# Kernel tuning notes

Measured on AMD Instinct MI355X. Metric: run time of the kernel, lower is better.

Reference implementation:

```python
import jax, jax.numpy as jnp
import numpy as np

B, N, P, K = 4, 8192, 2048, 16
C_IN, C_OUT, DIMS = 64, 128, 3
C_MID = C_OUT // 4                      # 32 (C_in != 0 branch)
DM = min(int(np.ceil(C_OUT / C_IN)), 4) # 2, depth multiplier for SepConv
C_DENSE = C_OUT // 2                    # 64, dense-projected feature dim
C_CAT = C_MID + C_DENSE                 # 96, lifted + projected features


def setup_inputs() -> dict:
    key = jax.random.key(0)
    ks = jax.random.split(key, 12)
    g = lambda k, shape, fan: jax.random.normal(k, shape, jnp.float32) / np.sqrt(fan).astype(np.float32)
    return {
        "pts": jax.random.normal(ks[0], (B, N, DIMS), jnp.float32),
        "fts": jax.random.normal(ks[1], (B, N, C_IN), jnp.float32),
        # PointCNN.dense: Linear(C_in, C_out//2) + ELU
        "dense_W": g(ks[2], (C_IN, C_DENSE), C_IN), "dense_b": jnp.zeros((C_DENSE,), jnp.float32),
        # XConv.dense1/dense2: Linear(dims,C_mid)+ELU, Linear(C_mid,C_mid)+ELU
        "d1_W": g(ks[3], (DIMS, C_MID), DIMS), "d1_b": jnp.zeros((C_MID,), jnp.float32),
        "d2_W": g(ks[4], (C_MID, C_MID), C_MID), "d2_b": jnp.zeros((C_MID,), jnp.float32),
        # conv2d: Conv2d(dims, K*K, (1,K)) + ELU, weight (out, in, kW)
        "conv_W": g(ks[5], (K * K, DIMS, K), DIMS * K), "conv_b": jnp.zeros((K * K,), jnp.float32),
        # dep_conv1/2: depthwise Conv2d(K, K*K, (1,K), groups=K); weight (group, mult, kW)
        "dw1_W": g(ks[6], (K, K, K), K), "dw1_b": jnp.zeros((K, K), jnp.float32),
        "dw2_W": g(ks[7], (K, K, K), K), "dw2_b": jnp.zeros((K, K), jnp.float32),
        # end_conv SepConv: depthwise (C_CAT groups, DM mult, (1,K)) then pointwise 1x1 -> C_OUT, ELU
        "sep_dw_W": g(ks[8], (C_CAT, DM, K), K), "sep_dw_b": jnp.zeros((C_CAT, DM), jnp.float32),
        "sep_pw_W": g(ks[9], (C_OUT, C_CAT, DM), C_CAT * DM), "sep_pw_b": jnp.zeros((C_OUT,), jnp.float32),
    }


def _fps(pts, npoint):
    """Iterative farthest point sampling (deterministic start at index 0)."""
    b, n, _ = pts.shape
    dist0 = jnp.full((b, n), 1e10, pts.dtype)
    far0 = jnp.zeros((b,), jnp.int32)

    def step(carry, _):
        dist, far = carry
        centroid = jnp.take_along_axis(pts, far[:, None, None], axis=1)  # [B,1,3]
        d = jnp.sum((pts - centroid) ** 2, -1)                            # [B,N]
        dist = jnp.minimum(dist, d)
        return (dist, jnp.argmax(dist, -1).astype(jnp.int32)), far

    _, idx = jax.lax.scan(step, (dist0, far0), None, length=npoint)  # [P,B]
    idx = idx.T                                                       # [B,P]
    return jnp.take_along_axis(pts, idx[..., None], axis=1)          # [B,P,3]


def reference(pts, fts, dense_W, dense_b, d1_W, d1_b, d2_W, d2_b,
              conv_W, conv_b, dw1_W, dw1_b, dw2_W, dw2_b,
              sep_dw_W, sep_dw_b, sep_pw_W, sep_pw_b):
    rep_pts = _fps(pts, P)                                            # [B,P,3]
    fts_d = jax.nn.elu(fts @ dense_W + dense_b)                       # [B,N,64]
    # KNN: squared distances rep->all points, K smallest
    d2 = (jnp.sum(rep_pts ** 2, -1)[..., None]
          - 2.0 * jnp.einsum('npc,nqc->npq', rep_pts, pts)
          + jnp.sum(pts ** 2, -1)[:, None, :])                        # [B,P,N]
    _, idx = jax.lax.top_k(-d2, K)                                    # [B,P,K]
    bidx = jnp.arange(B)[:, None, None]
    pts_reg = pts[bidx, idx]                                          # [B,P,K,3]
    fts_reg = fts_d[bidx, idx]                                        # [B,P,K,64]
    # XConv
    pl = pts_reg - rep_pts[:, :, None, :]                             # local coords
    lift = jax.nn.elu(jax.nn.elu(pl @ d1_W + d1_b) @ d2_W + d2_b)     # [B,P,K,C_MID]
    fts_cat = jnp.concatenate([lift, fts_reg], -1)                    # [B,P,K,C_CAT]
    X = jax.nn.elu(jnp.einsum('npkc,ock->npo', pl, conv_W) + conv_b).reshape(B, P, K, K)
    # depthwise convs over neighbor axis (spatial dim collapses to 1 -> einsum)
    X = jax.nn.elu(jnp.einsum('npij,jmi->npjm', X, dw1_W) + dw1_b)
    X = jnp.einsum('npij,jmi->npjm', X, dw2_W) + dw2_b
    fts_X = jnp.einsum('npab,npbc->npac', X, fts_cat)                 # [B,P,K,C_CAT]
    # separable end conv: depthwise over K, pointwise to C_OUT, ELU
    d = jnp.einsum('npkc,cmk->npcm', fts_X, sep_dw_W) + sep_dw_b
    fts_p = jax.nn.elu(jnp.einsum('npcm,ocm->npo', d, sep_pw_W) + sep_pw_b)  # [B,P,C_OUT]
    return rep_pts, fts_p
```

## Files before the change

### kernel.cpp

```cpp
#include <hip/hip_runtime.h>

#define BB 4
#define NN 8192
#define PP 2048
#define KNB 16
#define CIN 64
#define COUT 128

__device__ __forceinline__ float elu(float x) { return x > 0.0f ? x : expm1f(x); }

__device__ __forceinline__ unsigned fkey(float d) {
    unsigned u = __float_as_uint(d);
    unsigned m = (unsigned)((int)u >> 31);
    return u ^ (m | 0x80000000u);
}

__device__ __forceinline__ float wave_max_dpp(float v) {
#define DPP_STEP(ctrl)                                                         \
    {                                                                          \
        int x = __float_as_int(v);                                             \
        int y = __builtin_amdgcn_update_dpp(x, x, (ctrl), 0xf, 0xf, false);    \
        v = fmaxf(v, __int_as_float(y));                                       \
    }
    DPP_STEP(0x111)
    DPP_STEP(0x112)
    DPP_STEP(0x114)
    DPP_STEP(0x118)
    DPP_STEP(0x142)
    DPP_STEP(0x143)
#undef DPP_STEP
    return __int_as_float(__builtin_amdgcn_readlane(__float_as_int(v), 63));
}

__device__ __forceinline__ unsigned wave_min_u32_dpp(unsigned v) {
#define DPP_STEP(ctrl)                                                         \
    {                                                                          \
        int y = __builtin_amdgcn_update_dpp((int)v, (int)v, (ctrl), 0xf, 0xf, false); \
        v = min(v, (unsigned)y);                                               \
    }
    DPP_STEP(0x111)
    DPP_STEP(0x112)
    DPP_STEP(0x114)
    DPP_STEP(0x118)
    DPP_STEP(0x142)
    DPP_STEP(0x143)
#undef DPP_STEP
    return (unsigned)__builtin_amdgcn_readlane((int)v, 63);
}

#define PREP_BLOCKS 64
#define DENSE_BASE (4 + PREP_BLOCKS)
#define TOTAL_BLOCKS (DENSE_BASE + BB * NN / 8)

__global__ __launch_bounds__(512) void fps_kernel(
    const float* __restrict__ pts, float* __restrict__ rep,
    const float* __restrict__ fts, const float* __restrict__ denseW,
    const float* __restrict__ denseb, float* __restrict__ ftsd,
    const float* __restrict__ convW, const float* __restrict__ dw1W,
    const float* __restrict__ dw2W, const float* __restrict__ sdwW,
    const float* __restrict__ spwW,
    float* __restrict__ convT, float* __restrict__ dw1T, float* __restrict__ dw2T,
    float* __restrict__ sdwT, float* __restrict__ spwT, float* __restrict__ ptsT) {
    const int bid = blockIdx.x;
    const int t = threadIdx.x;

    __shared__ float spx[NN];
    __shared__ float spy[NN];
    __shared__ float spz[NN];
    __shared__ unsigned long long partk[2][8];

    if (bid >= DENSE_BASE) {
        const int row = (bid - DENSE_BASE) * 8 + (t >> 6);
        const int c = t & 63;
        float v = fts[(size_t)row * 64 + c];
        float acc = denseb[c];
#pragma unroll 8
        for (int k = 0; k < 64; ++k) acc = fmaf(__shfl(v, k), denseW[k * 64 + c], acc);
        ftsd[(size_t)row * 64 + c] = elu(acc);
        return;
    }
    if (bid >= 4) {
        int i = (bid - 4) * 512 + t;
        if (i < 12288) {
            int k = i & 15, c = (i >> 4) % 3, o = i / 48;
            convT[(c * 16 + k) * 256 + o] = convW[i];
        }
        if (i < 4096) {
            int ii = i & 15, e = i >> 4;
            dw1T[ii * 256 + e] = dw1W[i];
            dw2T[ii * 256 + e] = dw2W[i];
        }
        if (i < 3072) {
            int k = i & 15, e = i >> 4;
            sdwT[k * 192 + e] = sdwW[i];
        }
        if (i < 24576) {
            int e2 = i % 192, o = i / 192;
            spwT[e2 * 128 + o] = spwW[i];
        }
        {
            int j = i & 8191, b2 = i >> 13;
#pragma unroll
            for (int d = 0; d < 3; ++d)
                ptsT[((size_t)b2 * 3 + d) * NN + j] = pts[((size_t)b2 * NN + j) * 3 + d];
        }
        return;
    }

    const int b = bid;
    const int lane = t & 63, wave = t >> 6;

    const float* pb = pts + (size_t)b * NN * 3;
    for (int i = t; i < NN; i += 512) {
        spx[i] = pb[3 * i + 0];
        spy[i] = pb[3 * i + 1];
        spz[i] = pb[3 * i + 2];
    }
    __syncthreads();

    float px[16], py[16], pz[16], dist[16];
#pragma unroll
    for (int r = 0; r < 16; ++r) {
        px[r] = spx[t * 16 + r];
        py[r] = spy[t * 16 + r];
        pz[r] = spz[t * 16 + r];
        dist[r] = 1e10f;
    }

    float cx = spx[0], cy = spy[0], cz = spz[0];
    if (t == 0) {
        rep[(size_t)b * PP * 3 + 0] = cx;
        rep[(size_t)b * PP * 3 + 1] = cy;
        rep[(size_t)b * PP * 3 + 2] = cz;
    }

    int buf = 0;
    for (int s = 1; s < PP; ++s) {
        float bv = -1.0f; int bi = 0;
#pragma unroll
        for (int r = 0; r < 16; ++r) {
            float dx = __fsub_rn(px[r], cx);
            float dy = __fsub_rn(py[r], cy);
            float dz = __fsub_rn(pz[r], cz);
            float d = __fadd_rn(__fadd_rn(__fmul_rn(dx, dx), __fmul_rn(dy, dy)), __fmul_rn(dz, dz));
            float nd = fminf(dist[r], d);
            dist[r] = nd;
            bool tk = nd > bv;
            bi = tk ? (t * 16 + r) : bi;
            bv = fmaxf(nd, bv);
        }

        float wmax = wave_max_dpp(bv);
        unsigned long long mask = __ballot(bv == wmax);
        int wl = __ffsll(mask) - 1;
        int wbi = __shfl(bi, wl);

        if (lane == 0)
            partk[buf][wave] = ((unsigned long long)__float_as_uint(wmax) << 32)
                             | (unsigned)(8191 - wbi);
        __syncthreads();

        unsigned long long kk = partk[buf][0];
#pragma unroll
        for (int q = 1; q < 8; ++q) {
            unsigned long long c = partk[buf][q];
            kk = c > kk ? c : kk;
        }
        int widx = 8191 - (int)(unsigned)(kk & 0xFFFFFFFFULL);
        cx = spx[widx]; cy = spy[widx]; cz = spz[widx];
        if (t == 0) {
            float* rp = rep + ((size_t)b * PP + s) * 3;
            rp[0] = cx; rp[1] = cy; rp[2] = cz;
        }
        buf ^= 1;
    }
}

__global__ __launch_bounds__(256) void knn_kernel(const float* __restrict__ ptsT,
                                                  const float* __restrict__ rep,
                                                  int* __restrict__ kidx) {
    const int wid = blockIdx.x * 4 + (threadIdx.x >> 6);
    const int lane = threadIdx.x & 63;
    const int b = wid >> 11;
    const float* pxT = ptsT + (size_t)b * 3 * NN;
    const float* pyT = pxT + NN;
    const float* pzT = pxT + 2 * NN;

    float rx = rep[(size_t)wid * 3 + 0];
    float ry = rep[(size_t)wid * 3 + 1];
    float rz = rep[(size_t)wid * 3 + 2];
    float a = __fadd_rn(__fadd_rn(__fmul_rn(rx, rx), __fmul_rn(ry, ry)), __fmul_rn(rz, rz));

    unsigned long long key[16];
#pragma unroll
    for (int s = 0; s < 16; ++s) key[s] = ~0ULL;

    unsigned tau = 0xFFFFFFFFu;
    int it = 0;
    for (int j = lane; j < NN; j += 64, ++it) {
        float qx = pxT[j], qy = pyT[j], qz = pzT[j];
        float cc = __fadd_rn(__fadd_rn(__fmul_rn(qx, qx), __fmul_rn(qy, qy)), __fmul_rn(qz, qz));
        float bs = __fadd_rn(__fadd_rn(__fmul_rn(rx, qx), __fmul_rn(ry, qy)), __fmul_rn(rz, qz));
        float d2 = __fadd_rn(__fsub_rn(a, __fmul_rn(2.0f, bs)), cc);
        unsigned fk = fkey(d2);
        if (fk <= tau) {
            unsigned long long nk = ((unsigned long long)fk << 32) | (unsigned)j;
            if (nk < key[15]) {
                key[15] = nk;
#pragma unroll
                for (int s2 = 15; s2 > 0; --s2) {
                    unsigned long long u = key[s2 - 1], w = key[s2];
                    bool sw = w < u;
                    key[s2 - 1] = sw ? w : u;
                    key[s2] = sw ? u : w;
                }
            }
        }
        if ((it & 7) == 7)
            tau = wave_min_u32_dpp((unsigned)(key[15] >> 32));
    }

    int outv = 0;
#pragma unroll 1
    for (int r = 0; r < 16; ++r) {
        unsigned long long h = key[0];
#pragma unroll
        for (int off = 1; off < 64; off <<= 1) {
            unsigned long long o = __shfl_xor(h, off);
            h = (o < h) ? o : h;
        }
        if (lane == r) outv = (int)(unsigned)(h & 0xFFFFFFFFull);
        if (key[0] == h) {
#pragma unroll
            for (int s2 = 0; s2 < 15; ++s2) key[s2] = key[s2 + 1];
            key[15] = ~0ULL;
        }
    }
    if (lane < 16) kidx[(size_t)wid * 16 + lane] = outv;
}

__global__ __launch_bounds__(128) void xconv_kernel(
    const float* __restrict__ pts, const float* __restrict__ rep,
    const float* __restrict__ ftsd, const int* __restrict__ kidx,
    const float* __restrict__ d1W, const float* __restrict__ d1b,
    const float* __restrict__ d2W, const float* __restrict__ d2b,
    const float* __restrict__ convT, const float* __restrict__ convb,
    const float* __restrict__ dw1T, const float* __restrict__ dw1b,
    const float* __restrict__ dw2T, const float* __restrict__ dw2b,
    const float* __restrict__ sdwT, const float* __restrict__ sdwb,
    const float* __restrict__ spwT, const float* __restrict__ spwb,
    float* __restrict__ outp) {
    const int bp = blockIdx.x;
    const int b = bp >> 11;
    const int t = threadIdx.x;
    const int c64 = t & 63;

    __shared__ float pl[16][3];
    __shared__ int nidx[16];
    __shared__ float fcat[16][96];
    __shared__ float A1[16][32];
    __shared__ float Xm[16][17];
    __shared__ float X2[16][17];
    __shared__ float X3[16][17];
    __shared__ float fX[16][97];
    __shared__ float dsep[192];

    if (t < 16) {
        int id = kidx[(size_t)bp * 16 + t];
        nidx[t] = id;
        const float* q = pts + ((size_t)b * NN + id) * 3;
        const float* rr = rep + (size_t)bp * 3;
        pl[t][0] = q[0] - rr[0];
        pl[t][1] = q[1] - rr[1];
        pl[t][2] = q[2] - rr[2];
    }
    __syncthreads();

#pragma unroll
    for (int it = 0; it < 8; ++it) {
        int k = (t >> 6) + it * 2;
        fcat[k][32 + c64] = ftsd[((size_t)b * NN + nidx[k]) * 64 + c64];
    }

#pragma unroll
    for (int r2 = 0; r2 < 4; ++r2) {
        int e = t + 128 * r2; int k = e >> 5, j = e & 31;
        float acc = d1b[j];
        acc = fmaf(pl[k][0], d1W[j], acc);
        acc = fmaf(pl[k][1], d1W[32 + j], acc);
        acc = fmaf(pl[k][2], d1W[64 + j], acc);
        A1[k][j] = elu(acc);
    }
    __syncthreads();

#pragma unroll
    for (int r2 = 0; r2 < 4; ++r2) {
        int e = t + 128 * r2; int k = e >> 5, j = e & 31;
        float acc = d2b[j];
#pragma unroll
        for (int c = 0; c < 32; ++c) acc = fmaf(A1[k][c], d2W[c * 32 + j], acc);
        fcat[k][j] = elu(acc);
    }
    __syncthreads();

    {
        float a0 = convb[t], a1 = convb[t + 128];
#pragma unroll
        for (int c = 0; c < 3; ++c)
#pragma unroll
            for (int k = 0; k < 16; ++k) {
                float p = pl[k][c];
                const float* w = convT + (c * 16 + k) * 256 + t;
                a0 = fmaf(p, w[0],   a0);
                a1 = fmaf(p, w[128], a1);
            }
        Xm[t >> 4][t & 15] = elu(a0);
        Xm[(t >> 4) + 8][t & 15] = elu(a1);
    }
    __syncthreads();

    {
        int m = t & 15, j0 = t >> 4;
        float a0 = dw1b[t], a1 = dw1b[t + 128];
#pragma unroll
        for (int i = 0; i < 16; ++i) {
            const float* w = dw1T + i * 256 + t;
            a0 = fmaf(Xm[i][j0],     w[0],   a0);
            a1 = fmaf(Xm[i][j0 + 8], w[128], a1);
        }
        X2[j0][m] = elu(a0); X2[j0 + 8][m] = elu(a1);
    }
    __syncthreads();

    {
        int m = t & 15, j0 = t >> 4;
        float a0 = dw2b[t], a1 = dw2b[t + 128];
#pragma unroll
        for (int i = 0; i < 16; ++i) {
            const float* w = dw2T + i * 256 + t;
            a0 = fmaf(X2[i][j0],     w[0],   a0);
            a1 = fmaf(X2[i][j0 + 8], w[128], a1);
        }
        X3[j0][m] = a0; X3[j0 + 8][m] = a1;
    }
    __syncthreads();

#pragma unroll
    for (int r2 = 0; r2 < 12; ++r2) {
        int e = t + 128 * r2; int a = e & 15, c = e >> 4;
        float acc = 0.0f;
#pragma unroll
        for (int q = 0; q < 16; ++q) acc = fmaf(X3[a][q], fcat[q][c], acc);
        fX[a][c] = acc;
    }
    __syncthreads();

#pragma unroll
    for (int r2 = 0; r2 < 2; ++r2) {
        int e = t + 128 * r2;
        if (e < 192) {
            int c = e >> 1;
            float acc = sdwb[e];
#pragma unroll
            for (int k = 0; k < 16; ++k) acc = fmaf(fX[k][c], sdwT[k * 192 + e], acc);
            dsep[e] = acc;
        }
    }
    __syncthreads();

    {
        float a0 = spwb[t];
#pragma unroll 16
        for (int e2 = 0; e2 < 192; ++e2)
            a0 = fmaf(dsep[e2], spwT[e2 * 128 + t], a0);
        outp[(size_t)bp * 128 + t] = elu(a0);
    }
}

extern "C" void kernel_launch(void* const* d_in, const int* in_sizes, int n_in,
                              void* d_out, int out_size, void* d_ws, size_t ws_size,
                              hipStream_t stream) {
    const float* pts    = (const float*)d_in[0];
    const float* fts    = (const float*)d_in[1];
    const float* denseW = (const float*)d_in[2];
    const float* denseb = (const float*)d_in[3];
    const float* d1W    = (const float*)d_in[4];
    const float* d1b    = (const float*)d_in[5];
    const float* d2W    = (const float*)d_in[6];
    const float* d2b    = (const float*)d_in[7];
    const float* convW  = (const float*)d_in[8];
    const float* convb  = (const float*)d_in[9];
    const float* dw1W   = (const float*)d_in[10];
    const float* dw1b   = (const float*)d_in[11];
    const float* dw2W   = (const float*)d_in[12];
    const float* dw2b   = (const float*)d_in[13];
    const float* sdwW   = (const float*)d_in[14];
    const float* sdwb   = (const float*)d_in[15];
    const float* spwW   = (const float*)d_in[16];
    const float* spwb   = (const float*)d_in[17];

    float* rep  = (float*)d_out;
    float* outp = (float*)d_out + (size_t)BB * PP * 3;

    float* ftsd = (float*)d_ws;
    int*   kidx = (int*)((char*)d_ws + (size_t)BB * NN * CIN * sizeof(float));
    float* wts  = (float*)((char*)d_ws + (size_t)BB * NN * CIN * sizeof(float)
                                       + (size_t)BB * PP * KNB * sizeof(int));
    float* convT = wts;
    float* dw1T  = wts + 12288;
    float* dw2T  = wts + 16384;
    float* sdwT  = wts + 20480;
    float* spwT  = wts + 23552;
    float* ptsT  = wts + 48128;

    fps_kernel<<<TOTAL_BLOCKS, 512, 0, stream>>>(pts, rep, fts, denseW, denseb, ftsd,
                                                 convW, dw1W, dw2W, sdwW, spwW,
                                                 convT, dw1T, dw2T, sdwT, spwT, ptsT);
    knn_kernel<<<BB * PP / 4, 256, 0, stream>>>(ptsT, rep, kidx);
    xconv_kernel<<<BB * PP, 128, 0, stream>>>(pts, rep, ftsd, kidx,
                                              d1W, d1b, d2W, d2b, convT, convb,
                                              dw1T, dw1b, dw2T, dw2b,
                                              sdwT, sdwb, spwT, spwb, outp);
}
```

Before: 2.269 ms.

## Fuse kNN into XConv kernel and use atomicMax reduction in FPS loop

Merges the kNN search and the XConv computation into one kernel. Each 128-thread block runs kNN for two points, one wave each, keeps the neighbor indices in shared memory, then processes both points' XConv in sequence. This removes a kernel launch and the global round trip for the neighbor indices. The FPS per-step reduction now has each wave atomicMax into a rotating triple-buffered shared slot, replacing the per-wave partial array and serial 8-way scan. Risks include shared atomic contention and lower parallelism in the XConv phase, since there are half as many blocks.

```diff
diff --git a/kernel.cpp b/kernel.cpp
--- a/kernel.cpp
+++ b/kernel.cpp
@@ -67,7 +67,7 @@
     __shared__ float spx[NN];
     __shared__ float spy[NN];
     __shared__ float spz[NN];
-    __shared__ unsigned long long partk[2][8];
+    __shared__ unsigned long long slots[3];
 
     if (bid >= DENSE_BASE) {
         const int row = (bid - DENSE_BASE) * 8 + (t >> 6);
@@ -108,7 +108,7 @@
     }
 
     const int b = bid;
-    const int lane = t & 63, wave = t >> 6;
+    const int lane = t & 63;
 
     const float* pb = pts + (size_t)b * NN * 3;
     for (int i = t; i < NN; i += 512) {
@@ -116,6 +116,7 @@
         spy[i] = pb[3 * i + 1];
         spz[i] = pb[3 * i + 2];
     }
+    if (t < 3) slots[t] = 0ULL;
     __syncthreads();
 
     float px[16], py[16], pz[16], dist[16];
@@ -134,7 +135,7 @@
         rep[(size_t)b * PP * 3 + 2] = cz;
     }
 
-    int buf = 0;
+    int cur = 1;
     for (int s = 1; s < PP; ++s) {
         float bv = -1.0f; int bi = 0;
 #pragma unroll
@@ -155,93 +156,28 @@
         int wl = __ffsll(mask) - 1;
         int wbi = __shfl(bi, wl);
 
+        int nxt = (cur == 2) ? 0 : cur + 1;
         if (lane == 0)
-            partk[buf][wave] = ((unsigned long long)__float_as_uint(wmax) << 32)
-                             | (unsigned)(8191 - wbi);
-        __syncthreads();
-
-        unsigned long long kk = partk[buf][0];
-#pragma unroll
-        for (int q = 1; q < 8; ++q) {
-            unsigned long long c = partk[buf][q];
-            kk = c > kk ? c : kk;
-        }
+            atomicMax((unsigned long long*)&slots[cur],
+                      ((unsigned long long)__float_as_uint(wmax) << 32)
+                      | (unsigned)(8191 - wbi));
+        if (t == 0) slots[nxt] = 0ULL;
+        __syncthreads();
+
+        unsigned long long kk = slots[cur];
         int widx = 8191 - (int)(unsigned)(kk & 0xFFFFFFFFULL);
         cx = spx[widx]; cy = spy[widx]; cz = spz[widx];
         if (t == 0) {
             float* rp = rep + ((size_t)b * PP + s) * 3;
             rp[0] = cx; rp[1] = cy; rp[2] = cz;
         }
-        buf ^= 1;
-    }
-}
-
-__global__ __launch_bounds__(256) void knn_kernel(const float* __restrict__ ptsT,
-                                                  const float* __restrict__ rep,
-                                                  int* __restrict__ kidx) {
-    const int wid = blockIdx.x * 4 + (threadIdx.x >> 6);
-    const int lane = threadIdx.x & 63;
-    const int b = wid >> 11;
-    const float* pxT = ptsT + (size_t)b * 3 * NN;
-    const float* pyT = pxT + NN;
-    const float* pzT = pxT + 2 * NN;
-
-    float rx = rep[(size_t)wid * 3 + 0];
-    float ry = rep[(size_t)wid * 3 + 1];
-    float rz = rep[(size_t)wid * 3 + 2];
-    float a = __fadd_rn(__fadd_rn(__fmul_rn(rx, rx), __fmul_rn(ry, ry)), __fmul_rn(rz, rz));
-
-    unsigned long long key[16];
-#pragma unroll
-    for (int s = 0; s < 16; ++s) key[s] = ~0ULL;
-
-    unsigned tau = 0xFFFFFFFFu;
-    int it = 0;
-    for (int j = lane; j < NN; j += 64, ++it) {
-        float qx = pxT[j], qy = pyT[j], qz = pzT[j];
-        float cc = __fadd_rn(__fadd_rn(__fmul_rn(qx, qx), __fmul_rn(qy, qy)), __fmul_rn(qz, qz));
-        float bs = __fadd_rn(__fadd_rn(__fmul_rn(rx, qx), __fmul_rn(ry, qy)), __fmul_rn(rz, qz));
-        float d2 = __fadd_rn(__fsub_rn(a, __fmul_rn(2.0f, bs)), cc);
-        unsigned fk = fkey(d2);
-        if (fk <= tau) {
-            unsigned long long nk = ((unsigned long long)fk << 32) | (unsigned)j;
-            if (nk < key[15]) {
-                key[15] = nk;
-#pragma unroll
-                for (int s2 = 15; s2 > 0; --s2) {
-                    unsigned long long u = key[s2 - 1], w = key[s2];
-                    bool sw = w < u;
-                    key[s2 - 1] = sw ? w : u;
-                    key[s2] = sw ? u : w;
-                }
-            }
-        }
-        if ((it & 7) == 7)
-            tau = wave_min_u32_dpp((unsigned)(key[15] >> 32));
-    }
-
-    int outv = 0;
-#pragma unroll 1
-    for (int r = 0; r < 16; ++r) {
-        unsigned long long h = key[0];
-#pragma unroll
-        for (int off = 1; off < 64; off <<= 1) {
-            unsigned long long o = __shfl_xor(h, off);
-            h = (o < h) ? o : h;
-        }
-        if (lane == r) outv = (int)(unsigned)(h & 0xFFFFFFFFull);
-        if (key[0] == h) {
-#pragma unroll
-            for (int s2 = 0; s2 < 15; ++s2) key[s2] = key[s2 + 1];
-            key[15] = ~0ULL;
-        }
-    }
-    if (lane < 16) kidx[(size_t)wid * 16 + lane] = outv;
-}
-
-__global__ __launch_bounds__(128) void xconv_kernel(
-    const float* __restrict__ pts, const float* __restrict__ rep,
-    const float* __restrict__ ftsd, const int* __restrict__ kidx,
+        cur = nxt;
+    }
+}
+
+__global__ __launch_bounds__(128) void knnxconv_kernel(
+    const float* __restrict__ ptsT, const float* __restrict__ pts,
+    const float* __restrict__ rep, const float* __restrict__ ftsd,
     const float* __restrict__ d1W, const float* __restrict__ d1b,
     const float* __restrict__ d2W, const float* __restrict__ d2b,
     const float* __restrict__ convT, const float* __restrict__ convb,
@@ -250,11 +186,12 @@
     const float* __restrict__ sdwT, const float* __restrict__ sdwb,
     const float* __restrict__ spwT, const float* __restrict__ spwb,
     float* __restrict__ outp) {
-    const int bp = blockIdx.x;
-    const int b = bp >> 11;
+    const int blk = blockIdx.x;
     const int t = threadIdx.x;
+    const int wv = t >> 6, lane = t & 63;
     const int c64 = t & 63;
 
+    __shared__ int kidx_l[2][16];
     __shared__ float pl[16][3];
     __shared__ int nidx[16];
     __shared__ float fcat[16][96];
@@ -265,115 +202,182 @@
     __shared__ float fX[16][97];
     __shared__ float dsep[192];
 
-    if (t < 16) {
-        int id = kidx[(size_t)bp * 16 + t];
-        nidx[t] = id;
-        const float* q = pts + ((size_t)b * NN + id) * 3;
-        const float* rr = rep + (size_t)bp * 3;
-        pl[t][0] = q[0] - rr[0];
-        pl[t][1] = q[1] - rr[1];
-        pl[t][2] = q[2] - rr[2];
-    }
-    __syncthreads();
-
-#pragma unroll
-    for (int it = 0; it < 8; ++it) {
-        int k = (t >> 6) + it * 2;
-        fcat[k][32 + c64] = ftsd[((size_t)b * NN + nidx[k]) * 64 + c64];
-    }
-
-#pragma unroll
-    for (int r2 = 0; r2 < 4; ++r2) {
-        int e = t + 128 * r2; int k = e >> 5, j = e & 31;
-        float acc = d1b[j];
-        acc = fmaf(pl[k][0], d1W[j], acc);
-        acc = fmaf(pl[k][1], d1W[32 + j], acc);
-        acc = fmaf(pl[k][2], d1W[64 + j], acc);
-        A1[k][j] = elu(acc);
-    }
-    __syncthreads();
-
-#pragma unroll
-    for (int r2 = 0; r2 < 4; ++r2) {
-        int e = t + 128 * r2; int k = e >> 5, j = e & 31;
-        float acc = d2b[j];
-#pragma unroll
-        for (int c = 0; c < 32; ++c) acc = fmaf(A1[k][c], d2W[c * 32 + j], acc);
-        fcat[k][j] = elu(acc);
-    }
-    __syncthreads();
-
     {
-        float a0 = convb[t], a1 = convb[t + 128];
-#pragma unroll
-        for (int c = 0; c < 3; ++c)
-#pragma unroll
-            for (int k = 0; k < 16; ++k) {
-                float p = pl[k][c];
-                const float* w = convT + (c * 16 + k) * 256 + t;
-                a0 = fmaf(p, w[0],   a0);
-                a1 = fmaf(p, w[128], a1);
-            }
-        Xm[t >> 4][t & 15] = elu(a0);
-        Xm[(t >> 4) + 8][t & 15] = elu(a1);
-    }
-    __syncthreads();
-
-    {
-        int m = t & 15, j0 = t >> 4;
-        float a0 = dw1b[t], a1 = dw1b[t + 128];
-#pragma unroll
-        for (int i = 0; i < 16; ++i) {
-            const float* w = dw1T + i * 256 + t;
-            a0 = fmaf(Xm[i][j0],     w[0],   a0);
-            a1 = fmaf(Xm[i][j0 + 8], w[128], a1);
-        }
-        X2[j0][m] = elu(a0); X2[j0 + 8][m] = elu(a1);
-    }
-    __syncthreads();
-
-    {
-        int m = t & 15, j0 = t >> 4;
-        float a0 = dw2b[t], a1 = dw2b[t + 128];
-#pragma unroll
-        for (int i = 0; i < 16; ++i) {
-            const float* w = dw2T + i * 256 + t;
-            a0 = fmaf(X2[i][j0],     w[0],   a0);
-            a1 = fmaf(X2[i][j0 + 8], w[128], a1);
-        }
-        X3[j0][m] = a0; X3[j0 + 8][m] = a1;
-    }
-    __syncthreads();
-
-#pragma unroll
-    for (int r2 = 0; r2 < 12; ++r2) {
-        int e = t + 128 * r2; int a = e & 15, c = e >> 4;
-        float acc = 0.0f;
-#pragma unroll
-        for (int q = 0; q < 16; ++q) acc = fmaf(X3[a][q], fcat[q][c], acc);
-        fX[a][c] = acc;
-    }
-    __syncthreads();
-
-#pragma unroll
-    for (int r2 = 0; r2 < 2; ++r2) {
-        int e = t + 128 * r2;
-        if (e < 192) {
-            int c = e >> 1;
-            float acc = sdwb[e];
-#pragma unroll
-            for (int k = 0; k < 16; ++k) acc = fmaf(fX[k][c], sdwT[k * 192 + e], acc);
-            dsep[e] = acc;
-        }
-    }
-    __syncthreads();
-
-    {
-        float a0 = spwb[t];
+        const int wid = blk * 2 + wv;
+        const int b = wid >> 11;
+        const float* pxT = ptsT + (size_t)b * 3 * NN;
+        const float* pyT = pxT + NN;
+        const float* pzT = pxT + 2 * NN;
+
+        float rx = rep[(size_t)wid * 3 + 0];
+        float ry = rep[(size_t)wid * 3 + 1];
+        float rz = rep[(size_t)wid * 3 + 2];
+        float a = __fadd_rn(__fadd_rn(__fmul_rn(rx, rx), __fmul_rn(ry, ry)), __fmul_rn(rz, rz));
+
+        unsigned long long key[16];
+#pragma unroll
+        for (int s = 0; s < 16; ++s) key[s] = ~0ULL;
+
+        unsigned tau = 0xFFFFFFFFu;
+        int it = 0;
+        for (int j = lane; j < NN; j += 64, ++it) {
+            float qx = pxT[j], qy = pyT[j], qz = pzT[j];
+            float cc = __fadd_rn(__fadd_rn(__fmul_rn(qx, qx), __fmul_rn(qy, qy)), __fmul_rn(qz, qz));
+            float bs = __fadd_rn(__fadd_rn(__fmul_rn(rx, qx), __fmul_rn(ry, qy)), __fmul_rn(rz, qz));
+            float d2 = __fadd_rn(__fsub_rn(a, __fmul_rn(2.0f, bs)), cc);
+            unsigned fk = fkey(d2);
+            if (fk <= tau) {
+                unsigned long long nk = ((unsigned long long)fk << 32) | (unsigned)j;
+                if (nk < key[15]) {
+                    key[15] = nk;
+#pragma unroll
+                    for (int s2 = 15; s2 > 0; --s2) {
+                        unsigned long long u = key[s2 - 1], w = key[s2];
+                        bool sw = w < u;
+                        key[s2 - 1] = sw ? w : u;
+                        key[s2] = sw ? u : w;
+                    }
+                }
+            }
+            if ((it & 7) == 7)
+                tau = wave_min_u32_dpp((unsigned)(key[15] >> 32));
+        }
+
+        int outv = 0;
+#pragma unroll 1
+        for (int r = 0; r < 16; ++r) {
+            unsigned long long h = key[0];
+#pragma unroll
+            for (int off = 1; off < 64; off <<= 1) {
+                unsigned long long o = __shfl_xor(h, off);
+                h = (o < h) ? o : h;
+            }
+            if (lane == r) outv = (int)(unsigned)(h & 0xFFFFFFFFull);
+            if (key[0] == h) {
+#pragma unroll
+                for (int s2 = 0; s2 < 15; ++s2) key[s2] = key[s2 + 1];
+                key[15] = ~0ULL;
+            }
+        }
+        if (lane < 16) kidx_l[wv][lane] = outv;
+    }
+
+#pragma unroll 1
+    for (int pp = 0; pp < 2; ++pp) {
+        const int bp = blk * 2 + pp;
+        const int b = bp >> 11;
+        __syncthreads();
+
+        if (t < 16) {
+            int id = kidx_l[pp][t];
+            nidx[t] = id;
+            const float* q = pts + ((size_t)b * NN + id) * 3;
+            const float* rr = rep + (size_t)bp * 3;
+            pl[t][0] = q[0] - rr[0];
+            pl[t][1] = q[1] - rr[1];
+            pl[t][2] = q[2] - rr[2];
+        }
+        __syncthreads();
+
+#pragma unroll
+        for (int it = 0; it < 8; ++it) {
+            int k = (t >> 6) + it * 2;
+            fcat[k][32 + c64] = ftsd[((size_t)b * NN + nidx[k]) * 64 + c64];
+        }
+
+#pragma unroll
+        for (int r2 = 0; r2 < 4; ++r2) {
+            int e = t + 128 * r2; int k = e >> 5, j = e & 31;
+            float acc = d1b[j];
+            acc = fmaf(pl[k][0], d1W[j], acc);
+            acc = fmaf(pl[k][1], d1W[32 + j], acc);
+            acc = fmaf(pl[k][2], d1W[64 + j], acc);
+            A1[k][j] = elu(acc);
+        }
+        __syncthreads();
+
+#pragma unroll
+        for (int r2 = 0; r2 < 4; ++r2) {
+            int e = t + 128 * r2; int k = e >> 5, j = e & 31;
+            float acc = d2b[j];
+#pragma unroll
+            for (int c = 0; c < 32; ++c) acc = fmaf(A1[k][c], d2W[c * 32 + j], acc);
+            fcat[k][j] = elu(acc);
+        }
+        __syncthreads();
+
+        {
+            float a0 = convb[t], a1 = convb[t + 128];
+#pragma unroll
+            for (int c = 0; c < 3; ++c)
+#pragma unroll
+                for (int k = 0; k < 16; ++k) {
+                    float p = pl[k][c];
+                    const float* w = convT + (c * 16 + k) * 256 + t;
+                    a0 = fmaf(p, w[0],   a0);
+                    a1 = fmaf(p, w[128], a1);
+                }
+            Xm[t >> 4][t & 15] = elu(a0);
+            Xm[(t >> 4) + 8][t & 15] = elu(a1);
+        }
+        __syncthreads();
+
+        {
+            int m = t & 15, j0 = t >> 4;
+            float a0 = dw1b[t], a1 = dw1b[t + 128];
+#pragma unroll
+            for (int i = 0; i < 16; ++i) {
+                const float* w = dw1T + i * 256 + t;
+                a0 = fmaf(Xm[i][j0],     w[0],   a0);
+                a1 = fmaf(Xm[i][j0 + 8], w[128], a1);
+            }
+            X2[j0][m] = elu(a0); X2[j0 + 8][m] = elu(a1);
+        }
+        __syncthreads();
+
+        {
+            int m = t & 15, j0 = t >> 4;
+            float a0 = dw2b[t], a1 = dw2b[t + 128];
+#pragma unroll
+            for (int i = 0; i < 16; ++i) {
+                const float* w = dw2T + i * 256 + t;
+                a0 = fmaf(X2[i][j0],     w[0],   a0);
+                a1 = fmaf(X2[i][j0 + 8], w[128], a1);
+            }
+            X3[j0][m] = a0; X3[j0 + 8][m] = a1;
+        }
+        __syncthreads();
+
+#pragma unroll
+        for (int r2 = 0; r2 < 12; ++r2) {
+            int e = t + 128 * r2; int a = e & 15, c = e >> 4;
+            float acc = 0.0f;
+#pragma unroll
+            for (int q = 0; q < 16; ++q) acc = fmaf(X3[a][q], fcat[q][c], acc);
+            fX[a][c] = acc;
+        }
+        __syncthreads();
+
+#pragma unroll
+        for (int r2 = 0; r2 < 2; ++r2) {
+            int e = t + 128 * r2;
+            if (e < 192) {
+                int c = e >> 1;
+                float acc = sdwb[e];
+#pragma unroll
+                for (int k = 0; k < 16; ++k) acc = fmaf(fX[k][c], sdwT[k * 192 + e], acc);
+                dsep[e] = acc;
+            }
+        }
+        __syncthreads();
+
+        {
+            float a0 = spwb[t];
 #pragma unroll 16
-        for (int e2 = 0; e2 < 192; ++e2)
-            a0 = fmaf(dsep[e2], spwT[e2 * 128 + t], a0);
-        outp[(size_t)bp * 128 + t] = elu(a0);
+            for (int e2 = 0; e2 < 192; ++e2)
+                a0 = fmaf(dsep[e2], spwT[e2 * 128 + t], a0);
+            outp[(size_t)bp * 128 + t] = elu(a0);
+        }
     }
 }
 
@@ -403,7 +407,6 @@
     float* outp = (float*)d_out + (size_t)BB * PP * 3;
 
     float* ftsd = (float*)d_ws;
-    int*   kidx = (int*)((char*)d_ws + (size_t)BB * NN * CIN * sizeof(float));
     float* wts  = (float*)((char*)d_ws + (size_t)BB * NN * CIN * sizeof(float)
                                        + (size_t)BB * PP * KNB * sizeof(int));
     float* convT = wts;
@@ -416,9 +419,8 @@
     fps_kernel<<<TOTAL_BLOCKS, 512, 0, stream>>>(pts, rep, fts, denseW, denseb, ftsd,
                                                  convW, dw1W, dw2W, sdwW, spwW,
                                                  convT, dw1T, dw2T, sdwT, spwT, ptsT);
-    knn_kernel<<<BB * PP / 4, 256, 0, stream>>>(ptsT, rep, kidx);
-    xconv_kernel<<<BB * PP, 128, 0, stream>>>(pts, rep, ftsd, kidx,
-                                              d1W, d1b, d2W, d2b, convT, convb,
-                                              dw1T, dw1b, dw2T, dw2b,
-                                              sdwT, sdwb, spwT, spwb, outp);
-}
+    knnxconv_kernel<<<BB * PP / 2, 128, 0, stream>>>(ptsT, pts, rep, ftsd,
+                                                     d1W, d1b, d2W, d2b, convT, convb,
+                                                     dw1T, dw1b, dw2T, dw2b,
+                                                     sdwT, sdwb, spwT, spwb, outp);
+}
```

Result: slower. 3.223 ms (+42.1%).
